# Performance work log

Hardware: AMD Instinct MI355X
Metric: run time of the kernel (lower is better)

Reference implementation:

```python
import jax, jax.numpy as jnp
import numpy as np

B, G, N, D = 2, 2, 2048, 512
H, DH = 8, 64
DI = H * DH  # dim_inner = 512


def rmsnorm(x, gamma):
    # x: [b, g, n, d]; original normalizes over feature dim (F.normalize, eps=1e-12)
    norm = jnp.linalg.norm(x, axis=-1, keepdims=True)
    normed = x / jnp.maximum(norm, 1e-12)
    return normed * jnp.sqrt(jnp.asarray(x.shape[-1], x.dtype)) * gamma[None, :, None, :]


def setup_inputs() -> dict:
    key = jax.random.key(0)
    ks = jax.random.split(key, 8)
    x = jax.random.normal(ks[0], (B, G, N, D), dtype=jnp.float32)
    mask = jax.random.randint(ks[1], (B, N), 0, 2) > 0
    gamma_q = jnp.ones((G, D), dtype=jnp.float32)
    gamma_c = jnp.ones((G, D), dtype=jnp.float32)
    s = 0.02
    wq = jax.random.normal(ks[2], (G, DI, D), dtype=jnp.float32) * s
    wkv = jax.random.normal(ks[3], (G, 2 * DI, D), dtype=jnp.float32) * s
    wout = jax.random.normal(ks[4], (G, D, DI), dtype=jnp.float32) * s
    null_kv = jax.random.normal(ks[5], (2, G, H, 1, DH), dtype=jnp.float32)
    return {"x": x, "mask": mask, "gamma_q": gamma_q, "gamma_c": gamma_c,
            "wq": wq, "wkv": wkv, "wout": wout, "null_kv": null_kv}


def reference(x, mask, gamma_q, gamma_c, wq, wkv, wout, null_kv):
    b, g, n, d = x.shape
    # prenorm (context = x, so both norms applied to same input)
    xq = rmsnorm(x, gamma_q)
    xc = rmsnorm(x, gamma_c)
    # grouped 1x1 conv projections == per-group matmuls
    q = jnp.einsum('bgnd,ged->bgne', xq, wq)                 # [b,g,n,DI]
    kv = jnp.einsum('bgnd,ged->bgne', xc, wkv)               # [b,g,n,2*DI]
    k, v = jnp.split(kv, 2, axis=-1)
    def split_heads(t):
        return t.reshape(b, g, n, H, DH).transpose(0, 1, 3, 2, 4)  # [b,g,h,n,dh]
    q, k, v = map(split_heads, (q, k, v))
    # null kv: concat along sequence dim
    nk = jnp.broadcast_to(null_kv[0][None], (b, g, H, 1, DH))
    nv = jnp.broadcast_to(null_kv[1][None], (b, g, H, 1, DH))
    k = jnp.concatenate([nk, k], axis=-2)                    # [b,g,h,n+1,dh]
    v = jnp.concatenate([nv, v], axis=-2)
    # attention
    scale = DH ** -0.5
    scores = jnp.einsum('bghid,bghjd->bghij', q, k) * scale  # [b,g,h,n,n+1]
    m = jnp.concatenate([jnp.ones((b, 1), dtype=bool), mask], axis=-1)  # pad True for null kv
    scores = jnp.where(m[:, None, None, None, :], scores, jnp.asarray(-1e30, scores.dtype))
    attn = jax.nn.softmax(scores, axis=-1)
    out = jnp.einsum('bghij,bghjd->bghid', attn, v)          # [b,g,h,n,dh]
    out = out.transpose(0, 1, 3, 2, 4).reshape(b, g, n, DI)  # merge heads
    out = jnp.einsum('bgne,gde->bgnd', out, wout)
    return out
```

## Files before the change

kernel.cpp:

```cpp
#include <hip/hip_runtime.h>
#include <stdint.h>

typedef unsigned short u16;
typedef __attribute__((ext_vector_type(8))) short  bf16x8;
typedef __attribute__((ext_vector_type(8))) u16    u16x8;
typedef __attribute__((ext_vector_type(4))) u16    u16x4;
typedef __attribute__((ext_vector_type(4))) float  f32x4;
typedef __attribute__((ext_vector_type(2))) unsigned u32x2;

#define SEQ 2048
#define DIM 512
#define NH  8
#define NBG 4
#define QSCALE 0.18033688011112042f

__device__ __forceinline__ float bf2f(u16 u) { return __uint_as_float(((unsigned)u) << 16); }
__device__ __forceinline__ u16 f2bf(float f) {
  unsigned u = __float_as_uint(f);
  return (u16)((u + 0x7FFFu + ((u >> 16) & 1u)) >> 16);
}
__device__ __forceinline__ float h2f(u16 u) { return (float)__builtin_bit_cast(_Float16, u); }
__device__ __forceinline__ u16 f2h(float f) { return __builtin_bit_cast(unsigned short, (_Float16)f); }

__device__ __forceinline__ float ex2(float x) {
#if __has_builtin(__builtin_amdgcn_exp2f)
  return __builtin_amdgcn_exp2f(x);
#else
  return exp2f(x);
#endif
}

__device__ __forceinline__ void gload_lds16(const void* g, void* l) {
#if __has_builtin(__builtin_amdgcn_global_load_lds)
  __builtin_amdgcn_global_load_lds((__attribute__((address_space(1))) void*)g,
                                   (__attribute__((address_space(3))) void*)l, 16, 0, 0);
#else
  *(u16x8*)l = *(const u16x8*)g;
#endif
}

__device__ __forceinline__ int float_mode(const void* gq) {
  unsigned w0 = *(const unsigned*)gq;
  return (w0 == 0x3F800000u) ? 1 : ((w0 == 0x3C003C00u) ? 2 : 0);
}
__device__ __forceinline__ int mask_mode(const void* maskp) {
  const unsigned* mw = (const unsigned*)maskp;
  bool all01 = true, lowhit = false, f32ish = true;
#pragma unroll
  for (int i = 0; i < 64; i++) {
    unsigned v = mw[i];
    all01 = all01 && (v <= 1u);
    lowhit = lowhit || ((v & 0xFFFFu) == 0x3F80u) || ((v & 0xFFFFu) == 0x3C00u);
    f32ish = f32ish && (v == 0u || v == 0x3F800000u);
  }
  return all01 ? 0 : (lowhit ? 1 : (f32ish ? 2 : 3));
}
__device__ __forceinline__ bool mask_at(const void* m, int idx, int mode) {
  if (mode == 0) return ((const int*)m)[idx] != 0;
  if (mode == 1) return ((const u16*)m)[idx] != 0;
  if (mode == 2) return ((const float*)m)[idx] != 0.f;
  return ((const unsigned char*)m)[idx] != 0;
}
__device__ __forceinline__ float ldf(const void* p, int i, int mode) {
  if (mode == 1) return ((const float*)p)[i];
  if (mode == 2) return h2f(((const u16*)p)[i]);
  return bf2f(((const u16*)p)[i]);
}

__global__ __launch_bounds__(256) void pre_kernel(
    const void* __restrict__ x, const void* __restrict__ gq, const void* __restrict__ gc,
    const void* __restrict__ wq, const void* __restrict__ wkv, const void* __restrict__ wout,
    const void* __restrict__ nkv,
    u16* __restrict__ wqb, u16* __restrict__ wkvb, u16* __restrict__ woutb, u16* __restrict__ nkvb,
    u16* __restrict__ xn)
{
  const int NWQ = 2*512*512, NWKV = 2*1024*512, NWOUT = 2*512*512;
  int mode = float_mode(gq);
  if (blockIdx.x < 1025) {
    int loc = (blockIdx.x * 256 + threadIdx.x) * 8;
    const void* s; u16* d; int fold = 0; const void* gam = nullptr; int gbase = 0; float ex = 1.f;
    if (loc < NWQ) { s = wq; d = wqb; fold = 1; gam = gq; gbase = ((loc >> 18) << 9) | (loc & 511); ex = QSCALE; }
    else { loc -= NWQ;
      if (loc < NWKV) { s = wkv; d = wkvb; fold = 1; gam = gc; gbase = ((loc >> 19) << 9) | (loc & 511); }
      else { loc -= NWKV;
        if (loc < NWOUT) { s = wout; d = woutb; }
        else { loc -= NWOUT; if (loc < 2048) { s = nkv; d = nkvb; } else return; } } }
    u16x8 o;
#pragma unroll
    for (int j = 0; j < 8; j++) {
      float v = ldf(s, loc + j, mode) * ex;
      if (fold) v *= ldf(gam, gbase + j, mode);
      o[j] = f2bf(v);
    }
    *(u16x8*)(d + loc) = o;
    return;
  }
  int row  = (blockIdx.x - 1025) * 4 + (threadIdx.x >> 6);
  int lane = threadIdx.x & 63;
  float f[8];
  if (mode == 1) {
    const float* xr = (const float*)x + (size_t)row * DIM + lane * 8;
    f32x4 a = *(const f32x4*)xr, b2 = *(const f32x4*)(xr + 4);
#pragma unroll
    for (int i = 0; i < 4; i++) { f[i] = a[i]; f[i + 4] = b2[i]; }
  } else if (mode == 2) {
    u16x8 v = *(const u16x8*)((const u16*)x + (size_t)row * DIM + lane * 8);
#pragma unroll
    for (int i = 0; i < 8; i++) f[i] = h2f(v[i]);
  } else {
    u16x8 v = *(const u16x8*)((const u16*)x + (size_t)row * DIM + lane * 8);
#pragma unroll
    for (int i = 0; i < 8; i++) f[i] = bf2f(v[i]);
  }
  float ss = 0.f;
#pragma unroll
  for (int i = 0; i < 8; i++) ss += f[i] * f[i];
#pragma unroll
  for (int off = 32; off; off >>= 1) ss += __shfl_xor(ss, off);
  float scale = 22.62741699796952f / fmaxf(sqrtf(ss), 1e-12f);
  u16x8 o;
#pragma unroll
  for (int i = 0; i < 8; i++) o[i] = f2bf(f[i] * scale);
  *(u16x8*)(xn + (size_t)row * DIM + lane * 8) = o;
}

__global__ __launch_bounds__(256, 4) void gemm_qkv(
    const u16* __restrict__ A, const u16* __restrict__ wqb, const u16* __restrict__ wkvb,
    u16* __restrict__ qb, u16* __restrict__ kb, u16* __restrict__ vtb)
{
  __shared__ u16 As[128 * 64], Bs[64 * 64];
  int bg = blockIdx.z, g = bg & 1;
  int y = blockIdx.y;
  const u16* Bw; u16* C; u16* C2; int Ncols, splitcol, bn0;
  if (y < 8) { Bw = wqb;  C = qb; C2 = nullptr; Ncols = 512;  splitcol = 1 << 30; bn0 = y * 64; }
  else       { Bw = wkvb; C = kb; C2 = vtb;     Ncols = 1024; splitcol = 512;     bn0 = (y - 8) * 64; }
  const int M = SEQ, K = DIM, ldc = 512;
  int bm0 = blockIdx.x * 128;
  int tid = threadIdx.x, w = tid >> 6, l = tid & 63;
  int li = l & 15, lg = l >> 4;
  int wr = w >> 1, wc = w & 1;
  const u16* Ab = A + (size_t)bg * M * K;
  const u16* Bb = Bw + (size_t)g * Ncols * K;
  f32x4 acc[4][2];
#pragma unroll
  for (int m = 0; m < 4; m++)
#pragma unroll
    for (int n = 0; n < 2; n++) acc[m][n] = (f32x4){0.f, 0.f, 0.f, 0.f};
  for (int kt = 0; kt < K; kt += 64) {
#pragma unroll
    for (int i = 0; i < 4; i++) {
      int ch = i * 256 + tid;
      gload_lds16(Ab + (size_t)(bm0 + (ch >> 3)) * K + kt + ((ch & 7) << 3), &As[ch * 8]);
    }
#pragma unroll
    for (int i = 0; i < 2; i++) {
      int ch = i * 256 + tid;
      gload_lds16(Bb + (size_t)(bn0 + (ch >> 3)) * K + kt + ((ch & 7) << 3), &Bs[ch * 8]);
    }
    __syncthreads();
#pragma unroll
    for (int kk = 0; kk < 2; kk++) {
      bf16x8 a[4], b[2];
#pragma unroll
      for (int m = 0; m < 4; m++) a[m] = *(const bf16x8*)&As[(wr * 64 + m * 16 + li) * 64 + kk * 32 + lg * 8];
#pragma unroll
      for (int n = 0; n < 2; n++) b[n] = *(const bf16x8*)&Bs[(wc * 32 + n * 16 + li) * 64 + kk * 32 + lg * 8];
      __builtin_amdgcn_s_setprio(1);
#pragma unroll
      for (int m = 0; m < 4; m++)
#pragma unroll
        for (int n = 0; n < 2; n++)
          acc[m][n] = __builtin_amdgcn_mfma_f32_16x16x32_bf16(a[m], b[n], acc[m][n], 0, 0, 0);
      __builtin_amdgcn_s_setprio(0);
    }
    __syncthreads();
  }
#pragma unroll
  for (int m = 0; m < 4; m++) {
#pragma unroll
    for (int n = 0; n < 2; n++) {
      int row = bm0 + wr * 64 + m * 16 + lg * 4;
      int col = bn0 + wc * 32 + n * 16 + li;
      if (col < splitcol) {
        u16* cp = C + (size_t)bg * M * ldc + (size_t)row * ldc + col;
#pragma unroll
        for (int r = 0; r < 4; r++) cp[(size_t)r * ldc] = f2bf(acc[m][n][r]);
      } else {
        u16x4 pk;
#pragma unroll
        for (int r = 0; r < 4; r++) pk[r] = f2bf(acc[m][n][r]);
        *(u16x4*)&C2[(size_t)bg * 512 * M + (size_t)(col - 512) * M + row] = pk;
      }
    }
  }
}

__global__ __launch_bounds__(256, 4) void gemm_out(
    const u16* __restrict__ A, const u16* __restrict__ Bw,
    void* __restrict__ Cout, const void* __restrict__ gq0)
{
  __shared__ u16 As[128 * 64], Bs[64 * 64];
  const int M = SEQ, K = DIM, ldc = 512;
  int bg = blockIdx.z, g = bg & 1;
  int bm0 = blockIdx.x * 128, bn0 = blockIdx.y * 64;
  int tid = threadIdx.x, w = tid >> 6, l = tid & 63;
  int li = l & 15, lg = l >> 4;
  int wr = w >> 1, wc = w & 1;
  const u16* Ab = A + (size_t)bg * M * K;
  const u16* Bb = Bw + (size_t)g * 512 * K;
  f32x4 acc[4][2];
#pragma unroll
  for (int m = 0; m < 4; m++)
#pragma unroll
    for (int n = 0; n < 2; n++) acc[m][n] = (f32x4){0.f, 0.f, 0.f, 0.f};
  for (int kt = 0; kt < K; kt += 64) {
#pragma unroll
    for (int i = 0; i < 4; i++) {
      int ch = i * 256 + tid;
      gload_lds16(Ab + (size_t)(bm0 + (ch >> 3)) * K + kt + ((ch & 7) << 3), &As[ch * 8]);
    }
#pragma unroll
    for (int i = 0; i < 2; i++) {
      int ch = i * 256 + tid;
      gload_lds16(Bb + (size_t)(bn0 + (ch >> 3)) * K + kt + ((ch & 7) << 3), &Bs[ch * 8]);
    }
    __syncthreads();
#pragma unroll
    for (int kk = 0; kk < 2; kk++) {
      bf16x8 a[4], b[2];
#pragma unroll
      for (int m = 0; m < 4; m++) a[m] = *(const bf16x8*)&As[(wr * 64 + m * 16 + li) * 64 + kk * 32 + lg * 8];
#pragma unroll
      for (int n = 0; n < 2; n++) b[n] = *(const bf16x8*)&Bs[(wc * 32 + n * 16 + li) * 64 + kk * 32 + lg * 8];
      __builtin_amdgcn_s_setprio(1);
#pragma unroll
      for (int m = 0; m < 4; m++)
#pragma unroll
        for (int n = 0; n < 2; n++)
          acc[m][n] = __builtin_amdgcn_mfma_f32_16x16x32_bf16(a[m], b[n], acc[m][n], 0, 0, 0);
      __builtin_amdgcn_s_setprio(0);
    }
    __syncthreads();
  }
  int mode = float_mode(gq0);
#pragma unroll
  for (int m = 0; m < 4; m++) {
#pragma unroll
    for (int n = 0; n < 2; n++) {
      int row = bm0 + wr * 64 + m * 16 + lg * 4;
      int col = bn0 + wc * 32 + n * 16 + li;
      if (mode == 1) {
        float* cp = (float*)Cout + (size_t)bg * M * ldc + (size_t)row * ldc + col;
#pragma unroll
        for (int r = 0; r < 4; r++) cp[(size_t)r * ldc] = acc[m][n][r];
      } else if (mode == 2) {
        u16* cp = (u16*)Cout + (size_t)bg * M * ldc + (size_t)row * ldc + col;
#pragma unroll
        for (int r = 0; r < 4; r++) cp[(size_t)r * ldc] = f2h(acc[m][n][r]);
      } else {
        u16* cp = (u16*)Cout + (size_t)bg * M * ldc + (size_t)row * ldc + col;
#pragma unroll
        for (int r = 0; r < 4; r++) cp[(size_t)r * ldc] = f2bf(acc[m][n][r]);
      }
    }
  }
}

__global__ __launch_bounds__(256, 2) void attn_kernel(
    const u16* __restrict__ q, const u16* __restrict__ k, const u16* __restrict__ vt,
    const u16* __restrict__ nkv, const void* __restrict__ maskp, u16* __restrict__ ao)
{
  __shared__ __align__(16) u16 Kb[2][64 * 64];
  __shared__ __align__(16) u16 Vb[2][64 * 64];
  __shared__ __align__(16) u16 Ps[4][2][16 * 72];
  __shared__ __align__(4)  u16 mpk[SEQ];
  const int bid = blockIdx.x;
  const int h = bid & 7, bg = (bid >> 3) & 3, ib = bid >> 5;
  const int b = bg >> 1, g = bg & 1;
  const int tid = threadIdx.x, w = tid >> 6, l = tid & 63;
  const int li = l & 15, lg = l >> 4;
  const int i0 = ib * 128 + w * 32;

  auto stage = [&](int t, int buf) {
    int jb = t * 64;
#pragma unroll
    for (int p = 0; p < 2; p++) {
      int idx = p * 256 + tid;
      int j = idx >> 3, G = idx & 7;
      int c = (G ^ (j & 7)) << 3;
      gload_lds16(k + ((size_t)bg * SEQ + jb + j) * DIM + h * 64 + c, &Kb[buf][idx * 8]);
    }
#pragma unroll
    for (int p = 0; p < 2; p++) {
      int idx = p * 256 + tid;
      int d = idx >> 3, G = idx & 7;
      int c = (G ^ (d & 7)) << 3;
      gload_lds16(vt + ((size_t)bg * DIM + h * 64 + d) * SEQ + jb + c, &Vb[buf][idx * 8]);
    }
  };

  stage(0, 0);
  {
    const int smode = mask_mode(maskp);
#pragma unroll
    for (int i = 0; i < SEQ / 256; i++)
      mpk[i * 256 + tid] = mask_at(maskp, b * SEQ + i * 256 + tid, smode) ? 0xFFFFu : 0u;
  }

  bf16x8 qf[2][2];
#pragma unroll
  for (int rg = 0; rg < 2; rg++)
#pragma unroll
    for (int kk = 0; kk < 2; kk++)
      qf[rg][kk] = *(const bf16x8*)&q[((size_t)bg * SEQ + i0 + rg * 16 + li) * DIM + h * 64 + kk * 32 + lg * 8];

  bf16x8 ones;
#pragma unroll
  for (int r = 0; r < 8; r++) ones[r] = (short)0x3F80;

  const u16* nk = nkv + ((size_t)g * NH + h) * 64;
  const u16* nv = nkv + ((size_t)(2 + g) * NH + h) * 64;
  f32x4 oacc[2][4], lacc[2];
#pragma unroll
  for (int rg = 0; rg < 2; rg++) {
    float s = 0.f;
#pragma unroll
    for (int kk = 0; kk < 2; kk++)
#pragma unroll
      for (int r = 0; r < 8; r++)
        s += bf2f((u16)qf[rg][kk][r]) * bf2f(nk[kk * 32 + lg * 8 + r]);
    s += __shfl_xor(s, 16); s += __shfl_xor(s, 32);
    float pn = ex2(s);
    lacc[rg] = (f32x4){pn, pn, pn, pn};
#pragma unroll
    for (int dm = 0; dm < 4; dm++) {
      f32x4 o;
#pragma unroll
      for (int r = 0; r < 4; r++) o[r] = pn * bf2f(nv[dm * 16 + lg * 4 + r]);
      oacc[rg][dm] = o;
    }
  }
  __syncthreads();

  const int NT = SEQ / 64;
  for (int t = 0; t < NT; t++) {
    int cur = t & 1;
    if (t + 1 < NT) stage(t + 1, cur ^ 1);

    bf16x8 kf[4][2];
#pragma unroll
    for (int jm = 0; jm < 4; jm++)
#pragma unroll
      for (int kk = 0; kk < 2; kk++) {
        int gsw = ((kk * 4 + lg) ^ (li & 7)) << 3;
        kf[jm][kk] = *(const bf16x8*)&Kb[cur][(jm * 16 + li) * 64 + gsw];
      }

    f32x4 s4[2][4];
    __builtin_amdgcn_s_setprio(1);
#pragma unroll
    for (int rg = 0; rg < 2; rg++)
#pragma unroll
      for (int jm = 0; jm < 4; jm++) {
        f32x4 z = {0.f, 0.f, 0.f, 0.f};
        z = __builtin_amdgcn_mfma_f32_16x16x32_bf16(kf[jm][0], qf[rg][0], z, 0, 0, 0);
        z = __builtin_amdgcn_mfma_f32_16x16x32_bf16(kf[jm][1], qf[rg][1], z, 0, 0, 0);
        s4[rg][jm] = z;
      }
    __builtin_amdgcn_s_setprio(0);

    int jb = t * 64;
#pragma unroll
    for (int rg = 0; rg < 2; rg++) {
      u16* pb = &Ps[w][rg][0];
#pragma unroll
      for (int jm = 0; jm < 4; jm++) {
        unsigned u0 = __float_as_uint(ex2(s4[rg][jm][0]));
        unsigned u1 = __float_as_uint(ex2(s4[rg][jm][1]));
        unsigned u2 = __float_as_uint(ex2(s4[rg][jm][2]));
        unsigned u3 = __float_as_uint(ex2(s4[rg][jm][3]));
        unsigned mm01 = *(const unsigned*)&mpk[jb + jm * 16 + lg * 4];
        unsigned mm23 = *(const unsigned*)&mpk[jb + jm * 16 + lg * 4 + 2];
        unsigned w01 = __builtin_amdgcn_perm(u1, u0, 0x07060302u) & mm01;
        unsigned w23 = __builtin_amdgcn_perm(u3, u2, 0x07060302u) & mm23;
        *(u32x2*)&pb[li * 72 + jm * 16 + lg * 4] = (u32x2){w01, w23};
      }
    }

    bf16x8 vf[4][2];
#pragma unroll
    for (int jm = 0; jm < 4; jm++)
#pragma unroll
      for (int kk = 0; kk < 2; kk++) {
        int gsw = ((kk * 4 + lg) ^ (li & 7)) << 3;
        vf[jm][kk] = *(const bf16x8*)&Vb[cur][(jm * 16 + li) * 64 + gsw];
      }
#pragma unroll
    for (int rg = 0; rg < 2; rg++) {
      const u16* pb = &Ps[w][rg][0];
      bf16x8 pf0 = *(const bf16x8*)&pb[li * 72 + lg * 8];
      bf16x8 pf1 = *(const bf16x8*)&pb[li * 72 + 32 + lg * 8];
      __builtin_amdgcn_s_setprio(1);
      lacc[rg] = __builtin_amdgcn_mfma_f32_16x16x32_bf16(ones, pf0, lacc[rg], 0, 0, 0);
      lacc[rg] = __builtin_amdgcn_mfma_f32_16x16x32_bf16(ones, pf1, lacc[rg], 0, 0, 0);
#pragma unroll
      for (int dm = 0; dm < 4; dm++) {
        oacc[rg][dm] = __builtin_amdgcn_mfma_f32_16x16x32_bf16(vf[dm][0], pf0, oacc[rg][dm], 0, 0, 0);
        oacc[rg][dm] = __builtin_amdgcn_mfma_f32_16x16x32_bf16(vf[dm][1], pf1, oacc[rg][dm], 0, 0, 0);
      }
      __builtin_amdgcn_s_setprio(0);
    }
    __syncthreads();
  }
#pragma unroll
  for (int rg = 0; rg < 2; rg++) {
    float inv = 1.f / lacc[rg][0];
#pragma unroll
    for (int dm = 0; dm < 4; dm++) {
      u16x4 o;
#pragma unroll
      for (int r = 0; r < 4; r++) o[r] = f2bf(oacc[rg][dm][r] * inv);
      *(u16x4*)&ao[((size_t)bg * SEQ + i0 + rg * 16 + li) * DIM + h * 64 + dm * 16 + lg * 4] = o;
    }
  }
}

extern "C" void kernel_launch(void* const* d_in, const int* in_sizes, int n_in,
                              void* d_out, int out_size, void* d_ws, size_t ws_size,
                              hipStream_t stream) {
  const void* x    = d_in[0];
  const void* msk  = d_in[1];
  const void* gq   = d_in[2];
  const void* gc   = d_in[3];
  const void* wq   = d_in[4];
  const void* wkv  = d_in[5];
  const void* wout = d_in[6];
  const void* nkv  = d_in[7];

  u16* base = (u16*)d_ws;
  const size_t SLOT = (size_t)NBG * SEQ * DIM;
  u16* xn = base + 0 * SLOT;
  u16* ao = base + 0 * SLOT;
  u16* qb = base + 1 * SLOT;
  u16* kb = base + 2 * SLOT;
  u16* vt = base + 3 * SLOT;
  u16* wreg = base + 4 * SLOT;
  const int NWQ = 2 * 512 * 512, NWKV = 2 * 1024 * 512, NWOUT = 2 * 512 * 512;
  u16* wqb   = wreg;
  u16* wkvb  = wreg + NWQ;
  u16* woutb = wreg + NWQ + NWKV;
  u16* nkvb  = wreg + NWQ + NWKV + NWOUT;

  hipLaunchKernelGGL(pre_kernel, dim3(3073), dim3(256), 0, stream,
                     x, gq, gc, wq, wkv, wout, nkv, wqb, wkvb, woutb, nkvb, xn);
  hipLaunchKernelGGL(gemm_qkv, dim3(16, 24, NBG), dim3(256), 0, stream,
                     xn, wqb, wkvb, qb, kb, vt);
  hipLaunchKernelGGL(attn_kernel, dim3(512), dim3(256), 0, stream,
                     qb, kb, vt, nkvb, msk, ao);
  hipLaunchKernelGGL(gemm_out, dim3(16, 8, NBG), dim3(256), 0, stream,
                     ao, woutb, d_out, gq);
}
```

Baseline: 104.2 us.

## Switch attention to 32x32x16 MFMA and keep P in registers

Rewrites the attention inner loop to use 32x32x16 bf16 MFMA tiles instead of 16x16x32. The layout is chosen so the softmax probabilities produced by the QK^T MFMA can feed the PV MFMA directly from registers, which removes the per-wave shared-memory P staging buffer along with its writes and reads. V fragments are now assembled from two 8-byte LDS reads, and the loop is manually unrolled by two with explicit K/V double buffers. Larger accumulators raise register pressure, and the split V loads add LDS instructions.

```diff
diff --git a/kernel.cpp b/kernel.cpp
--- a/kernel.cpp
+++ b/kernel.cpp
@@ -6,7 +6,9 @@
 typedef __attribute__((ext_vector_type(8))) u16    u16x8;
 typedef __attribute__((ext_vector_type(4))) u16    u16x4;
 typedef __attribute__((ext_vector_type(4))) float  f32x4;
+typedef __attribute__((ext_vector_type(16))) float f32x16;
 typedef __attribute__((ext_vector_type(2))) unsigned u32x2;
+typedef __attribute__((ext_vector_type(4))) unsigned u32x4;
 
 #define SEQ 2048
 #define DIM 512
@@ -270,36 +272,37 @@
     const u16* __restrict__ q, const u16* __restrict__ k, const u16* __restrict__ vt,
     const u16* __restrict__ nkv, const void* __restrict__ maskp, u16* __restrict__ ao)
 {
-  __shared__ __align__(16) u16 Kb[2][64 * 64];
-  __shared__ __align__(16) u16 Vb[2][64 * 64];
-  __shared__ __align__(16) u16 Ps[4][2][16 * 72];
-  __shared__ __align__(4)  u16 mpk[SEQ];
+  __shared__ __align__(16) u16 Kb0[64 * 64], Kb1[64 * 64];
+  __shared__ __align__(16) u16 Vb0[64 * 64], Vb1[64 * 64];
+  __shared__ __align__(16) u16 mpk[SEQ];
   const int bid = blockIdx.x;
   const int h = bid & 7, bg = (bid >> 3) & 3, ib = bid >> 5;
   const int b = bg >> 1, g = bg & 1;
   const int tid = threadIdx.x, w = tid >> 6, l = tid & 63;
-  const int li = l & 15, lg = l >> 4;
+  const int lo = l & 31, hi = l >> 5;
+  const int dl7 = lo & 7;
   const int i0 = ib * 128 + w * 32;
-
-  auto stage = [&](int t, int buf) {
+  const unsigned* mpk32 = (const unsigned*)mpk;
+
+  auto stage = [&](int t, u16* kd, u16* vd) {
     int jb = t * 64;
 #pragma unroll
     for (int p = 0; p < 2; p++) {
       int idx = p * 256 + tid;
-      int j = idx >> 3, G = idx & 7;
-      int c = (G ^ (j & 7)) << 3;
-      gload_lds16(k + ((size_t)bg * SEQ + jb + j) * DIM + h * 64 + c, &Kb[buf][idx * 8]);
+      int r = idx >> 3, G = idx & 7;
+      int c = (G ^ (r & 7)) << 3;
+      gload_lds16(k + ((size_t)bg * SEQ + jb + r) * DIM + h * 64 + c, &kd[idx * 8]);
     }
 #pragma unroll
     for (int p = 0; p < 2; p++) {
       int idx = p * 256 + tid;
-      int d = idx >> 3, G = idx & 7;
-      int c = (G ^ (d & 7)) << 3;
-      gload_lds16(vt + ((size_t)bg * DIM + h * 64 + d) * SEQ + jb + c, &Vb[buf][idx * 8]);
+      int r = idx >> 3, G = idx & 7;
+      int c = (G ^ (r & 7)) << 3;
+      gload_lds16(vt + ((size_t)bg * DIM + h * 64 + r) * SEQ + jb + c, &vd[idx * 8]);
     }
   };
 
-  stage(0, 0);
+  stage(0, Kb0, Vb0);
   {
     const int smode = mask_mode(maskp);
 #pragma unroll
@@ -307,12 +310,10 @@
       mpk[i * 256 + tid] = mask_at(maskp, b * SEQ + i * 256 + tid, smode) ? 0xFFFFu : 0u;
   }
 
-  bf16x8 qf[2][2];
-#pragma unroll
-  for (int rg = 0; rg < 2; rg++)
-#pragma unroll
-    for (int kk = 0; kk < 2; kk++)
-      qf[rg][kk] = *(const bf16x8*)&q[((size_t)bg * SEQ + i0 + rg * 16 + li) * DIM + h * 64 + kk * 32 + lg * 8];
+  bf16x8 qf[4];
+#pragma unroll
+  for (int ks = 0; ks < 4; ks++)
+    qf[ks] = *(const bf16x8*)&q[((size_t)bg * SEQ + i0 + lo) * DIM + h * 64 + ks * 16 + hi * 8];
 
   bf16x8 ones;
 #pragma unroll
@@ -320,109 +321,95 @@
 
   const u16* nk = nkv + ((size_t)g * NH + h) * 64;
   const u16* nv = nkv + ((size_t)(2 + g) * NH + h) * 64;
-  f32x4 oacc[2][4], lacc[2];
-#pragma unroll
-  for (int rg = 0; rg < 2; rg++) {
-    float s = 0.f;
-#pragma unroll
-    for (int kk = 0; kk < 2; kk++)
-#pragma unroll
-      for (int r = 0; r < 8; r++)
-        s += bf2f((u16)qf[rg][kk][r]) * bf2f(nk[kk * 32 + lg * 8 + r]);
-    s += __shfl_xor(s, 16); s += __shfl_xor(s, 32);
-    float pn = ex2(s);
-    lacc[rg] = (f32x4){pn, pn, pn, pn};
-#pragma unroll
-    for (int dm = 0; dm < 4; dm++) {
-      f32x4 o;
-#pragma unroll
-      for (int r = 0; r < 4; r++) o[r] = pn * bf2f(nv[dm * 16 + lg * 4 + r]);
-      oacc[rg][dm] = o;
-    }
+  f32x16 oacc[2], lacc;
+  {
+    float s0 = 0.f;
+#pragma unroll
+    for (int ks = 0; ks < 4; ks++)
+#pragma unroll
+      for (int e = 0; e < 8; e++)
+        s0 += bf2f((u16)qf[ks][e]) * bf2f(nk[ks * 16 + hi * 8 + e]);
+    s0 += __shfl_xor(s0, 32);
+    float pn = ex2(s0);
+#pragma unroll
+    for (int r = 0; r < 16; r++) lacc[r] = pn;
+#pragma unroll
+    for (int dblk = 0; dblk < 2; dblk++)
+#pragma unroll
+      for (int r = 0; r < 16; r++)
+        oacc[dblk][r] = pn * bf2f(nv[dblk * 32 + (r & 3) + 8 * (r >> 2) + 4 * hi]);
   }
   __syncthreads();
 
+  auto tile = [&](const u16* kb, const u16* vb, int t) {
+    bf16x8 vf[2][4];
+#pragma unroll
+    for (int dblk = 0; dblk < 2; dblk++)
+#pragma unroll
+      for (int f = 0; f < 4; f++) {
+        int rowoff = (dblk * 32 + lo) * 64;
+        u32x2 c1 = *(const u32x2*)&vb[rowoff + (((2 * f)     ^ dl7) << 3) + 4 * hi];
+        u32x2 c2 = *(const u32x2*)&vb[rowoff + (((2 * f + 1) ^ dl7) << 3) + 4 * hi];
+        vf[dblk][f] = __builtin_bit_cast(bf16x8, (u32x4){c1[0], c1[1], c2[0], c2[1]});
+      }
+    unsigned U[2][4][2];
+#pragma unroll
+    for (int jblk = 0; jblk < 2; jblk++) {
+      f32x16 s;
+#pragma unroll
+      for (int r = 0; r < 16; r++) s[r] = 0.f;
+      __builtin_amdgcn_s_setprio(1);
+#pragma unroll
+      for (int ks = 0; ks < 4; ks++) {
+        bf16x8 kf = *(const bf16x8*)&kb[(jblk * 32 + lo) * 64 + (((ks * 2 + hi) ^ dl7) << 3)];
+        s = __builtin_amdgcn_mfma_f32_32x32x16_bf16(kf, qf[ks], s, 0, 0, 0);
+      }
+      __builtin_amdgcn_s_setprio(0);
+#pragma unroll
+      for (int a = 0; a < 4; a++) {
+        u32x2 mm = *(const u32x2*)&mpk32[t * 32 + jblk * 16 + a * 4 + hi * 2];
+        unsigned e0 = __float_as_uint(ex2(s[4 * a + 0]));
+        unsigned e1 = __float_as_uint(ex2(s[4 * a + 1]));
+        unsigned e2 = __float_as_uint(ex2(s[4 * a + 2]));
+        unsigned e3 = __float_as_uint(ex2(s[4 * a + 3]));
+        U[jblk][a][0] = __builtin_amdgcn_perm(e1, e0, 0x07060302u) & mm[0];
+        U[jblk][a][1] = __builtin_amdgcn_perm(e3, e2, 0x07060302u) & mm[1];
+      }
+    }
+    __builtin_amdgcn_s_setprio(1);
+#pragma unroll
+    for (int jblk = 0; jblk < 2; jblk++)
+#pragma unroll
+      for (int m = 0; m < 2; m++) {
+        bf16x8 pf = __builtin_bit_cast(bf16x8,
+          (u32x4){U[jblk][2 * m][0], U[jblk][2 * m][1], U[jblk][2 * m + 1][0], U[jblk][2 * m + 1][1]});
+        lacc    = __builtin_amdgcn_mfma_f32_32x32x16_bf16(ones, pf, lacc, 0, 0, 0);
+        oacc[0] = __builtin_amdgcn_mfma_f32_32x32x16_bf16(vf[0][jblk * 2 + m], pf, oacc[0], 0, 0, 0);
+        oacc[1] = __builtin_amdgcn_mfma_f32_32x32x16_bf16(vf[1][jblk * 2 + m], pf, oacc[1], 0, 0, 0);
+      }
+    __builtin_amdgcn_s_setprio(0);
+  };
+
   const int NT = SEQ / 64;
-  for (int t = 0; t < NT; t++) {
-    int cur = t & 1;
-    if (t + 1 < NT) stage(t + 1, cur ^ 1);
-
-    bf16x8 kf[4][2];
-#pragma unroll
-    for (int jm = 0; jm < 4; jm++)
-#pragma unroll
-      for (int kk = 0; kk < 2; kk++) {
-        int gsw = ((kk * 4 + lg) ^ (li & 7)) << 3;
-        kf[jm][kk] = *(const bf16x8*)&Kb[cur][(jm * 16 + li) * 64 + gsw];
-      }
-
-    f32x4 s4[2][4];
-    __builtin_amdgcn_s_setprio(1);
-#pragma unroll
-    for (int rg = 0; rg < 2; rg++)
-#pragma unroll
-      for (int jm = 0; jm < 4; jm++) {
-        f32x4 z = {0.f, 0.f, 0.f, 0.f};
-        z = __builtin_amdgcn_mfma_f32_16x16x32_bf16(kf[jm][0], qf[rg][0], z, 0, 0, 0);
-        z = __builtin_amdgcn_mfma_f32_16x16x32_bf16(kf[jm][1], qf[rg][1], z, 0, 0, 0);
-        s4[rg][jm] = z;
-      }
-    __builtin_amdgcn_s_setprio(0);
-
-    int jb = t * 64;
-#pragma unroll
-    for (int rg = 0; rg < 2; rg++) {
-      u16* pb = &Ps[w][rg][0];
-#pragma unroll
-      for (int jm = 0; jm < 4; jm++) {
-        unsigned u0 = __float_as_uint(ex2(s4[rg][jm][0]));
-        unsigned u1 = __float_as_uint(ex2(s4[rg][jm][1]));
-        unsigned u2 = __float_as_uint(ex2(s4[rg][jm][2]));
-        unsigned u3 = __float_as_uint(ex2(s4[rg][jm][3]));
-        unsigned mm01 = *(const unsigned*)&mpk[jb + jm * 16 + lg * 4];
-        unsigned mm23 = *(const unsigned*)&mpk[jb + jm * 16 + lg * 4 + 2];
-        unsigned w01 = __builtin_amdgcn_perm(u1, u0, 0x07060302u) & mm01;
-        unsigned w23 = __builtin_amdgcn_perm(u3, u2, 0x07060302u) & mm23;
-        *(u32x2*)&pb[li * 72 + jm * 16 + lg * 4] = (u32x2){w01, w23};
-      }
-    }
-
-    bf16x8 vf[4][2];
-#pragma unroll
-    for (int jm = 0; jm < 4; jm++)
-#pragma unroll
-      for (int kk = 0; kk < 2; kk++) {
-        int gsw = ((kk * 4 + lg) ^ (li & 7)) << 3;
-        vf[jm][kk] = *(const bf16x8*)&Vb[cur][(jm * 16 + li) * 64 + gsw];
-      }
-#pragma unroll
-    for (int rg = 0; rg < 2; rg++) {
-      const u16* pb = &Ps[w][rg][0];
-      bf16x8 pf0 = *(const bf16x8*)&pb[li * 72 + lg * 8];
-      bf16x8 pf1 = *(const bf16x8*)&pb[li * 72 + 32 + lg * 8];
-      __builtin_amdgcn_s_setprio(1);
-      lacc[rg] = __builtin_amdgcn_mfma_f32_16x16x32_bf16(ones, pf0, lacc[rg], 0, 0, 0);
-      lacc[rg] = __builtin_amdgcn_mfma_f32_16x16x32_bf16(ones, pf1, lacc[rg], 0, 0, 0);
-#pragma unroll
-      for (int dm = 0; dm < 4; dm++) {
-        oacc[rg][dm] = __builtin_amdgcn_mfma_f32_16x16x32_bf16(vf[dm][0], pf0, oacc[rg][dm], 0, 0, 0);
-        oacc[rg][dm] = __builtin_amdgcn_mfma_f32_16x16x32_bf16(vf[dm][1], pf1, oacc[rg][dm], 0, 0, 0);
-      }
-      __builtin_amdgcn_s_setprio(0);
-    }
-    __syncthreads();
-  }
-#pragma unroll
-  for (int rg = 0; rg < 2; rg++) {
-    float inv = 1.f / lacc[rg][0];
-#pragma unroll
-    for (int dm = 0; dm < 4; dm++) {
+  for (int t = 0; t < NT; t += 2) {
+    stage(t + 1, Kb1, Vb1);
+    tile(Kb0, Vb0, t);
+    __syncthreads();
+    if (t + 2 < NT) stage(t + 2, Kb0, Vb0);
+    tile(Kb1, Vb1, t + 1);
+    __syncthreads();
+  }
+
+  float inv = 1.f / lacc[0];
+#pragma unroll
+  for (int dblk = 0; dblk < 2; dblk++)
+#pragma unroll
+    for (int rq = 0; rq < 4; rq++) {
       u16x4 o;
 #pragma unroll
-      for (int r = 0; r < 4; r++) o[r] = f2bf(oacc[rg][dm][r] * inv);
-      *(u16x4*)&ao[((size_t)bg * SEQ + i0 + rg * 16 + li) * DIM + h * 64 + dm * 16 + lg * 4] = o;
-    }
-  }
+      for (int qq = 0; qq < 4; qq++) o[qq] = f2bf(oacc[dblk][4 * rq + qq] * inv);
+      *(u16x4*)&ao[((size_t)bg * SEQ + i0 + lo) * DIM + h * 64 + dblk * 32 + 8 * rq + 4 * hi] = o;
+    }
 }
 
 extern "C" void kernel_launch(void* const* d_in, const int* in_sizes, int n_in,
```

Measured after the change: 111.7 us. +7.2%, slower.

## Triple-buffer K/V tiles with prefetch distance two and explicit vmcnt waits

Applied to the files above, without the earlier changes.

The attention kernel moves from double-buffered to triple-buffered K/V LDS tiles and prefetches two tiles ahead. The full __syncthreads at each iteration is replaced by s_waitcnt vmcnt(4) plus s_barrier, so only the older tile's global-to-LDS loads must have landed. V fragment reads are hoisted before the softmax/P write, and the per-wave P scratch is cut to one 16x72 buffer reused across row groups. This aims to hide global load latency behind MFMA work, at the cost of more LDS (roughly 61 KB per block), which could limit occupancy, and of hand-written wait counts that must match the number of issued loads.

```diff
diff --git a/kernel.cpp b/kernel.cpp
--- a/kernel.cpp
+++ b/kernel.cpp
@@ -270,10 +270,10 @@
     const u16* __restrict__ q, const u16* __restrict__ k, const u16* __restrict__ vt,
     const u16* __restrict__ nkv, const void* __restrict__ maskp, u16* __restrict__ ao)
 {
-  __shared__ __align__(16) u16 Kb[2][64 * 64];
-  __shared__ __align__(16) u16 Vb[2][64 * 64];
-  __shared__ __align__(16) u16 Ps[4][2][16 * 72];
-  __shared__ __align__(4)  u16 mpk[SEQ];
+  __shared__ __align__(16) u16 KbAll[3 * 64 * 64];
+  __shared__ __align__(16) u16 VbAll[3 * 64 * 64];
+  __shared__ __align__(16) u16 Ps[4][16 * 72];
+  __shared__ __align__(16) u16 mpk[SEQ];
   const int bid = blockIdx.x;
   const int h = bid & 7, bg = (bid >> 3) & 3, ib = bid >> 5;
   const int b = bg >> 1, g = bg & 1;
@@ -283,23 +283,26 @@
 
   auto stage = [&](int t, int buf) {
     int jb = t * 64;
+    u16* kd = &KbAll[buf * 4096];
+    u16* vd = &VbAll[buf * 4096];
 #pragma unroll
     for (int p = 0; p < 2; p++) {
       int idx = p * 256 + tid;
-      int j = idx >> 3, G = idx & 7;
-      int c = (G ^ (j & 7)) << 3;
-      gload_lds16(k + ((size_t)bg * SEQ + jb + j) * DIM + h * 64 + c, &Kb[buf][idx * 8]);
+      int r = idx >> 3, G = idx & 7;
+      int c = (G ^ (r & 7)) << 3;
+      gload_lds16(k + ((size_t)bg * SEQ + jb + r) * DIM + h * 64 + c, &kd[idx * 8]);
     }
 #pragma unroll
     for (int p = 0; p < 2; p++) {
       int idx = p * 256 + tid;
-      int d = idx >> 3, G = idx & 7;
-      int c = (G ^ (d & 7)) << 3;
-      gload_lds16(vt + ((size_t)bg * DIM + h * 64 + d) * SEQ + jb + c, &Vb[buf][idx * 8]);
+      int r = idx >> 3, G = idx & 7;
+      int c = (G ^ (r & 7)) << 3;
+      gload_lds16(vt + ((size_t)bg * DIM + h * 64 + r) * SEQ + jb + c, &vd[idx * 8]);
     }
   };
 
   stage(0, 0);
+  stage(1, 1);
   {
     const int smode = mask_mode(maskp);
 #pragma unroll
@@ -340,12 +343,18 @@
       oacc[rg][dm] = o;
     }
   }
-  __syncthreads();
+  __builtin_amdgcn_sched_barrier(0);
+  asm volatile("s_waitcnt vmcnt(4) lgkmcnt(0)" ::: "memory");
+  __builtin_amdgcn_s_barrier();
+  __builtin_amdgcn_sched_barrier(0);
 
   const int NT = SEQ / 64;
   for (int t = 0; t < NT; t++) {
-    int cur = t & 1;
-    if (t + 1 < NT) stage(t + 1, cur ^ 1);
+    int cur = t % 3;
+    const u16* kbuf = &KbAll[cur * 4096];
+    const u16* vbuf = &VbAll[cur * 4096];
+    if (t + 2 < NT) stage(t + 2, (t + 2) % 3);
+    __builtin_amdgcn_sched_barrier(0);
 
     bf16x8 kf[4][2];
 #pragma unroll
@@ -353,7 +362,7 @@
 #pragma unroll
       for (int kk = 0; kk < 2; kk++) {
         int gsw = ((kk * 4 + lg) ^ (li & 7)) << 3;
-        kf[jm][kk] = *(const bf16x8*)&Kb[cur][(jm * 16 + li) * 64 + gsw];
+        kf[jm][kk] = *(const bf16x8*)&kbuf[(jm * 16 + li) * 64 + gsw];
       }
 
     f32x4 s4[2][4];
@@ -369,10 +378,19 @@
       }
     __builtin_amdgcn_s_setprio(0);
 
+    bf16x8 vf[4][2];
+#pragma unroll
+    for (int jm = 0; jm < 4; jm++)
+#pragma unroll
+      for (int kk = 0; kk < 2; kk++) {
+        int gsw = ((kk * 4 + lg) ^ (li & 7)) << 3;
+        vf[jm][kk] = *(const bf16x8*)&vbuf[(jm * 16 + li) * 64 + gsw];
+      }
+
     int jb = t * 64;
+    u16* pb = &Ps[w][0];
 #pragma unroll
     for (int rg = 0; rg < 2; rg++) {
-      u16* pb = &Ps[w][rg][0];
 #pragma unroll
       for (int jm = 0; jm < 4; jm++) {
         unsigned u0 = __float_as_uint(ex2(s4[rg][jm][0]));
@@ -385,19 +403,6 @@
         unsigned w23 = __builtin_amdgcn_perm(u3, u2, 0x07060302u) & mm23;
         *(u32x2*)&pb[li * 72 + jm * 16 + lg * 4] = (u32x2){w01, w23};
       }
-    }
-
-    bf16x8 vf[4][2];
-#pragma unroll
-    for (int jm = 0; jm < 4; jm++)
-#pragma unroll
-      for (int kk = 0; kk < 2; kk++) {
-        int gsw = ((kk * 4 + lg) ^ (li & 7)) << 3;
-        vf[jm][kk] = *(const bf16x8*)&Vb[cur][(jm * 16 + li) * 64 + gsw];
-      }
-#pragma unroll
-    for (int rg = 0; rg < 2; rg++) {
-      const u16* pb = &Ps[w][rg][0];
       bf16x8 pf0 = *(const bf16x8*)&pb[li * 72 + lg * 8];
       bf16x8 pf1 = *(const bf16x8*)&pb[li * 72 + 32 + lg * 8];
       __builtin_amdgcn_s_setprio(1);
@@ -410,8 +415,14 @@
       }
       __builtin_amdgcn_s_setprio(0);
     }
-    __syncthreads();
-  }
+
+    __builtin_amdgcn_sched_barrier(0);
+    if (t + 2 < NT) asm volatile("s_waitcnt vmcnt(4)" ::: "memory");
+    else            asm volatile("s_waitcnt vmcnt(0)" ::: "memory");
+    __builtin_amdgcn_s_barrier();
+    __builtin_amdgcn_sched_barrier(0);
+  }
+
 #pragma unroll
   for (int rg = 0; rg < 2; rg++) {
     float inv = 1.f / lacc[rg][0];
```

Result: slower. 107.0 us (+2.6%).

## Split attention query tile across 8 waves of 16 rows each

Applied to the files above, without the earlier changes.

The attention kernel now launches 512 threads per block, with each wave handling 16 query rows instead of 32. K/V staging uses one load per thread, and P-tile shared memory is resized to one buffer per wave. This halves per-wave register state and adds waves to hide latency. In exchange, each wave reuses each K/V fragment load for only one row group, so shared-memory read traffic per MFMA doubles.

```diff
diff --git a/kernel.cpp b/kernel.cpp
--- a/kernel.cpp
+++ b/kernel.cpp
@@ -266,36 +266,28 @@
   }
 }
 
-__global__ __launch_bounds__(256, 2) void attn_kernel(
+__global__ __launch_bounds__(512, 2) void attn_kernel(
     const u16* __restrict__ q, const u16* __restrict__ k, const u16* __restrict__ vt,
     const u16* __restrict__ nkv, const void* __restrict__ maskp, u16* __restrict__ ao)
 {
   __shared__ __align__(16) u16 Kb[2][64 * 64];
   __shared__ __align__(16) u16 Vb[2][64 * 64];
-  __shared__ __align__(16) u16 Ps[4][2][16 * 72];
-  __shared__ __align__(4)  u16 mpk[SEQ];
+  __shared__ __align__(16) u16 Ps[8][16 * 72];
+  __shared__ __align__(16) u16 mpk[SEQ];
   const int bid = blockIdx.x;
   const int h = bid & 7, bg = (bid >> 3) & 3, ib = bid >> 5;
   const int b = bg >> 1, g = bg & 1;
   const int tid = threadIdx.x, w = tid >> 6, l = tid & 63;
   const int li = l & 15, lg = l >> 4;
-  const int i0 = ib * 128 + w * 32;
+  const int i0 = ib * 128 + w * 16;
 
   auto stage = [&](int t, int buf) {
     int jb = t * 64;
-#pragma unroll
-    for (int p = 0; p < 2; p++) {
-      int idx = p * 256 + tid;
-      int j = idx >> 3, G = idx & 7;
-      int c = (G ^ (j & 7)) << 3;
-      gload_lds16(k + ((size_t)bg * SEQ + jb + j) * DIM + h * 64 + c, &Kb[buf][idx * 8]);
-    }
-#pragma unroll
-    for (int p = 0; p < 2; p++) {
-      int idx = p * 256 + tid;
-      int d = idx >> 3, G = idx & 7;
-      int c = (G ^ (d & 7)) << 3;
-      gload_lds16(vt + ((size_t)bg * DIM + h * 64 + d) * SEQ + jb + c, &Vb[buf][idx * 8]);
+    {
+      int r = tid >> 3, G = tid & 7;
+      int c = (G ^ (r & 7)) << 3;
+      gload_lds16(k + ((size_t)bg * SEQ + jb + r) * DIM + h * 64 + c, &Kb[buf][tid * 8]);
+      gload_lds16(vt + ((size_t)bg * DIM + h * 64 + r) * SEQ + jb + c, &Vb[buf][tid * 8]);
     }
   };
 
@@ -303,16 +295,14 @@
   {
     const int smode = mask_mode(maskp);
 #pragma unroll
-    for (int i = 0; i < SEQ / 256; i++)
-      mpk[i * 256 + tid] = mask_at(maskp, b * SEQ + i * 256 + tid, smode) ? 0xFFFFu : 0u;
-  }
-
-  bf16x8 qf[2][2];
-#pragma unroll
-  for (int rg = 0; rg < 2; rg++)
-#pragma unroll
-    for (int kk = 0; kk < 2; kk++)
-      qf[rg][kk] = *(const bf16x8*)&q[((size_t)bg * SEQ + i0 + rg * 16 + li) * DIM + h * 64 + kk * 32 + lg * 8];
+    for (int i = 0; i < SEQ / 512; i++)
+      mpk[i * 512 + tid] = mask_at(maskp, b * SEQ + i * 512 + tid, smode) ? 0xFFFFu : 0u;
+  }
+
+  bf16x8 qf[2];
+#pragma unroll
+  for (int kk = 0; kk < 2; kk++)
+    qf[kk] = *(const bf16x8*)&q[((size_t)bg * SEQ + i0 + li) * DIM + h * 64 + kk * 32 + lg * 8];
 
   bf16x8 ones;
 #pragma unroll
@@ -320,24 +310,23 @@
 
   const u16* nk = nkv + ((size_t)g * NH + h) * 64;
   const u16* nv = nkv + ((size_t)(2 + g) * NH + h) * 64;
-  f32x4 oacc[2][4], lacc[2];
-#pragma unroll
-  for (int rg = 0; rg < 2; rg++) {
+  f32x4 oacc[4], lacc;
+  {
     float s = 0.f;
 #pragma unroll
     for (int kk = 0; kk < 2; kk++)
 #pragma unroll
       for (int r = 0; r < 8; r++)
-        s += bf2f((u16)qf[rg][kk][r]) * bf2f(nk[kk * 32 + lg * 8 + r]);
+        s += bf2f((u16)qf[kk][r]) * bf2f(nk[kk * 32 + lg * 8 + r]);
     s += __shfl_xor(s, 16); s += __shfl_xor(s, 32);
     float pn = ex2(s);
-    lacc[rg] = (f32x4){pn, pn, pn, pn};
+    lacc = (f32x4){pn, pn, pn, pn};
 #pragma unroll
     for (int dm = 0; dm < 4; dm++) {
       f32x4 o;
 #pragma unroll
       for (int r = 0; r < 4; r++) o[r] = pn * bf2f(nv[dm * 16 + lg * 4 + r]);
-      oacc[rg][dm] = o;
+      oacc[dm] = o;
     }
   }
   __syncthreads();
@@ -356,36 +345,16 @@
         kf[jm][kk] = *(const bf16x8*)&Kb[cur][(jm * 16 + li) * 64 + gsw];
       }
 
-    f32x4 s4[2][4];
+    f32x4 s4[4];
     __builtin_amdgcn_s_setprio(1);
 #pragma unroll
-    for (int rg = 0; rg < 2; rg++)
-#pragma unroll
-      for (int jm = 0; jm < 4; jm++) {
-        f32x4 z = {0.f, 0.f, 0.f, 0.f};
-        z = __builtin_amdgcn_mfma_f32_16x16x32_bf16(kf[jm][0], qf[rg][0], z, 0, 0, 0);
-        z = __builtin_amdgcn_mfma_f32_16x16x32_bf16(kf[jm][1], qf[rg][1], z, 0, 0, 0);
-        s4[rg][jm] = z;
-      }
+    for (int jm = 0; jm < 4; jm++) {
+      f32x4 z = {0.f, 0.f, 0.f, 0.f};
+      z = __builtin_amdgcn_mfma_f32_16x16x32_bf16(kf[jm][0], qf[0], z, 0, 0, 0);
+      z = __builtin_amdgcn_mfma_f32_16x16x32_bf16(kf[jm][1], qf[1], z, 0, 0, 0);
+      s4[jm] = z;
+    }
     __builtin_amdgcn_s_setprio(0);
-
-    int jb = t * 64;
-#pragma unroll
-    for (int rg = 0; rg < 2; rg++) {
-      u16* pb = &Ps[w][rg][0];
-#pragma unroll
-      for (int jm = 0; jm < 4; jm++) {
-        unsigned u0 = __float_as_uint(ex2(s4[rg][jm][0]));
-        unsigned u1 = __float_as_uint(ex2(s4[rg][jm][1]));
-        unsigned u2 = __float_as_uint(ex2(s4[rg][jm][2]));
-        unsigned u3 = __float_as_uint(ex2(s4[rg][jm][3]));
-        unsigned mm01 = *(const unsigned*)&mpk[jb + jm * 16 + lg * 4];
-        unsigned mm23 = *(const unsigned*)&mpk[jb + jm * 16 + lg * 4 + 2];
-        unsigned w01 = __builtin_amdgcn_perm(u1, u0, 0x07060302u) & mm01;
-        unsigned w23 = __builtin_amdgcn_perm(u3, u2, 0x07060302u) & mm23;
-        *(u32x2*)&pb[li * 72 + jm * 16 + lg * 4] = (u32x2){w01, w23};
-      }
-    }
 
     bf16x8 vf[4][2];
 #pragma unroll
@@ -395,33 +364,42 @@
         int gsw = ((kk * 4 + lg) ^ (li & 7)) << 3;
         vf[jm][kk] = *(const bf16x8*)&Vb[cur][(jm * 16 + li) * 64 + gsw];
       }
-#pragma unroll
-    for (int rg = 0; rg < 2; rg++) {
-      const u16* pb = &Ps[w][rg][0];
-      bf16x8 pf0 = *(const bf16x8*)&pb[li * 72 + lg * 8];
-      bf16x8 pf1 = *(const bf16x8*)&pb[li * 72 + 32 + lg * 8];
-      __builtin_amdgcn_s_setprio(1);
-      lacc[rg] = __builtin_amdgcn_mfma_f32_16x16x32_bf16(ones, pf0, lacc[rg], 0, 0, 0);
-      lacc[rg] = __builtin_amdgcn_mfma_f32_16x16x32_bf16(ones, pf1, lacc[rg], 0, 0, 0);
-#pragma unroll
-      for (int dm = 0; dm < 4; dm++) {
-        oacc[rg][dm] = __builtin_amdgcn_mfma_f32_16x16x32_bf16(vf[dm][0], pf0, oacc[rg][dm], 0, 0, 0);
-        oacc[rg][dm] = __builtin_amdgcn_mfma_f32_16x16x32_bf16(vf[dm][1], pf1, oacc[rg][dm], 0, 0, 0);
-      }
-      __builtin_amdgcn_s_setprio(0);
-    }
+
+    int jb = t * 64;
+    u16* pb = &Ps[w][0];
+#pragma unroll
+    for (int jm = 0; jm < 4; jm++) {
+      unsigned u0 = __float_as_uint(ex2(s4[jm][0]));
+      unsigned u1 = __float_as_uint(ex2(s4[jm][1]));
+      unsigned u2 = __float_as_uint(ex2(s4[jm][2]));
+      unsigned u3 = __float_as_uint(ex2(s4[jm][3]));
+      unsigned mm01 = *(const unsigned*)&mpk[jb + jm * 16 + lg * 4];
+      unsigned mm23 = *(const unsigned*)&mpk[jb + jm * 16 + lg * 4 + 2];
+      unsigned w01 = __builtin_amdgcn_perm(u1, u0, 0x07060302u) & mm01;
+      unsigned w23 = __builtin_amdgcn_perm(u3, u2, 0x07060302u) & mm23;
+      *(u32x2*)&pb[li * 72 + jm * 16 + lg * 4] = (u32x2){w01, w23};
+    }
+    bf16x8 pf0 = *(const bf16x8*)&pb[li * 72 + lg * 8];
+    bf16x8 pf1 = *(const bf16x8*)&pb[li * 72 + 32 + lg * 8];
+    __builtin_amdgcn_s_setprio(1);
+    lacc = __builtin_amdgcn_mfma_f32_16x16x32_bf16(ones, pf0, lacc, 0, 0, 0);
+    lacc = __builtin_amdgcn_mfma_f32_16x16x32_bf16(ones, pf1, lacc, 0, 0, 0);
+#pragma unroll
+    for (int dm = 0; dm < 4; dm++) {
+      oacc[dm] = __builtin_amdgcn_mfma_f32_16x16x32_bf16(vf[dm][0], pf0, oacc[dm], 0, 0, 0);
+      oacc[dm] = __builtin_amdgcn_mfma_f32_16x16x32_bf16(vf[dm][1], pf1, oacc[dm], 0, 0, 0);
+    }
+    __builtin_amdgcn_s_setprio(0);
     __syncthreads();
   }
-#pragma unroll
-  for (int rg = 0; rg < 2; rg++) {
-    float inv = 1.f / lacc[rg][0];
-#pragma unroll
-    for (int dm = 0; dm < 4; dm++) {
-      u16x4 o;
-#pragma unroll
-      for (int r = 0; r < 4; r++) o[r] = f2bf(oacc[rg][dm][r] * inv);
-      *(u16x4*)&ao[((size_t)bg * SEQ + i0 + rg * 16 + li) * DIM + h * 64 + dm * 16 + lg * 4] = o;
-    }
+
+  float inv = 1.f / lacc[0];
+#pragma unroll
+  for (int dm = 0; dm < 4; dm++) {
+    u16x4 o;
+#pragma unroll
+    for (int r = 0; r < 4; r++) o[r] = f2bf(oacc[dm][r] * inv);
+    *(u16x4*)&ao[((size_t)bg * SEQ + i0 + li) * DIM + h * 64 + dm * 16 + lg * 4] = o;
   }
 }
 
@@ -455,7 +433,7 @@
                      x, gq, gc, wq, wkv, wout, nkv, wqb, wkvb, woutb, nkvb, xn);
   hipLaunchKernelGGL(gemm_qkv, dim3(16, 24, NBG), dim3(256), 0, stream,
                      xn, wqb, wkvb, qb, kb, vt);
-  hipLaunchKernelGGL(attn_kernel, dim3(512), dim3(256), 0, stream,
+  hipLaunchKernelGGL(attn_kernel, dim3(512), dim3(512), 0, stream,
                      qb, kb, vt, nkvb, msk, ao);
   hipLaunchKernelGGL(gemm_out, dim3(16, 8, NBG), dim3(256), 0, stream,
                      ao, woutb, d_out, gq);
```

Measured after the change: 107.6 us. +3.3%, slower.
